# Performance work log

Hardware: AMD Instinct MI355X
Metric: run time of the kernel (lower is better)

## Reference

```python
import jax, jax.numpy as jnp
import numpy as np

NUM_EXPERTS = 8
IN_FEATURES = 1024
OUT_FEATURES = 1024
TOP_K = 2


def setup_inputs() -> dict:
    key = jax.random.key(0)
    k_x, k_we, k_be, k_wg, k_bg = jax.random.split(key, 5)
    scale_e = 1.0 / np.sqrt(IN_FEATURES)
    x = jax.random.normal(k_x, (4, 2048, IN_FEATURES), dtype=jnp.float32)
    # expert weights stored torch-style [E, out, in], bias [E, out]
    W_experts = jax.random.uniform(k_we, (NUM_EXPERTS, OUT_FEATURES, IN_FEATURES), minval=-scale_e, maxval=scale_e, dtype=jnp.float32)
    b_experts = jax.random.uniform(k_be, (NUM_EXPERTS, OUT_FEATURES), minval=-scale_e, maxval=scale_e, dtype=jnp.float32)
    W_gate = jax.random.uniform(k_wg, (NUM_EXPERTS, IN_FEATURES), minval=-scale_e, maxval=scale_e, dtype=jnp.float32)
    b_gate = jax.random.uniform(k_bg, (NUM_EXPERTS,), minval=-scale_e, maxval=scale_e, dtype=jnp.float32)
    return {"x": x, "W_experts": W_experts, "b_experts": b_experts, "W_gate": W_gate, "b_gate": b_gate}


def reference(x, W_experts, b_experts, W_gate, b_gate):
    B, S, D = x.shape
    x_flat = x.reshape(-1, D)  # [T, D]
    # gating
    gate_logits = x_flat @ W_gate.T + b_gate  # [T, E]
    topk_vals, topk_idxs = jax.lax.top_k(gate_logits, TOP_K)  # [T, K]
    topk_weights = jax.nn.softmax(topk_vals, axis=-1)  # [T, K]
    # dense per-token per-expert weight via one-hot scatter of top-k weights
    one_hot = jax.nn.one_hot(topk_idxs, NUM_EXPERTS, dtype=x.dtype)  # [T, K, E]
    w = jnp.einsum('tke,tk->te', one_hot, topk_weights)  # [T, E]
    # every expert runs densely over all tokens (faithful to source)
    expert_outs = jnp.einsum('td,efd->tef', x_flat, W_experts) + b_experts  # [T, E, F]
    out_flat = jnp.einsum('te,tef->tf', w, expert_outs)  # [T, F]
    return out_flat.reshape(B, S, -1)
```

## Files before the change

### kernel.cpp

```cpp
#include <hip/hip_runtime.h>
#include <hip/hip_bf16.h>
#include <stdint.h>

#define NE 8
#define DK 1024
#define FN 1024
#define NTOK 8192

#define BM 320
#define BN 256
#define BK 64
#define NIT (DK / BK)
#define MT 52

#define HB 32
#define EPB (NTOK * 2 / HB)

#define BUFS 73728
#define BOFF 40960

typedef __attribute__((ext_vector_type(4))) float f32x4;
typedef __attribute__((ext_vector_type(8))) short short8;
typedef __attribute__((ext_vector_type(4))) short short4v;

__device__ __forceinline__ unsigned short f2bf(float f) {
    union { float f; unsigned u; } v; v.f = f;
    unsigned r = v.u;
    unsigned lsb = (r >> 16) & 1u;
    r += 0x7fffu + lsb;
    return (unsigned short)(r >> 16);
}
__device__ __forceinline__ float bf2f(unsigned short u) {
    union { unsigned u; float f; } v; v.u = ((unsigned)u) << 16;
    return v.f;
}

__global__ __launch_bounds__(256) void k_gate(const float* __restrict__ x,
    const float* __restrict__ Wg, const float* __restrict__ bg,
    unsigned short* __restrict__ xb, int* __restrict__ meta_e,
    float* __restrict__ meta_w)
{
    const int lane = threadIdx.x & 63;
    const int t = blockIdx.x * 4 + (threadIdx.x >> 6);

    const f32x4* xr = (const f32x4*)(x + (size_t)t * DK);
    f32x4 xv[4];
#pragma unroll
    for (int c = 0; c < 4; ++c) xv[c] = xr[lane + 64 * c];

    short4v* xbo = (short4v*)(xb + (size_t)t * DK);
#pragma unroll
    for (int c = 0; c < 4; ++c) {
        short4v b;
        b.x = (short)f2bf(xv[c].x); b.y = (short)f2bf(xv[c].y);
        b.z = (short)f2bf(xv[c].z); b.w = (short)f2bf(xv[c].w);
        xbo[lane + 64 * c] = b;
    }

    float acc[NE];
#pragma unroll
    for (int e = 0; e < NE; ++e) {
        const f32x4* wr = (const f32x4*)(Wg + e * DK);
        float a = 0.f;
#pragma unroll
        for (int c = 0; c < 4; ++c) {
            f32x4 wv = wr[lane + 64 * c];
            a += xv[c].x * wv.x + xv[c].y * wv.y + xv[c].z * wv.z + xv[c].w * wv.w;
        }
        acc[e] = a;
    }
#pragma unroll
    for (int e = 0; e < NE; ++e) {
        float a = acc[e];
#pragma unroll
        for (int off = 32; off > 0; off >>= 1) a += __shfl_xor(a, off, 64);
        acc[e] = a;
    }
    if (lane == 0) {
        float v[NE];
#pragma unroll
        for (int e = 0; e < NE; ++e) v[e] = acc[e] + bg[e];
        int b0 = 0; float m0 = v[0];
#pragma unroll
        for (int e = 1; e < NE; ++e) if (v[e] > m0) { m0 = v[e]; b0 = e; }
        int b1 = -1; float m1 = -3.4e38f;
#pragma unroll
        for (int e = 0; e < NE; ++e) if (e != b0 && v[e] > m1) { m1 = v[e]; b1 = e; }
        float r = expf(m1 - m0);
        float s = 1.f + r;
        meta_e[2 * t] = b0; meta_e[2 * t + 1] = b1;
        meta_w[2 * t] = 1.f / s; meta_w[2 * t + 1] = r / s;
    }
}

__global__ __launch_bounds__(256) void k_convw(const float* __restrict__ W,
                                               unsigned short* __restrict__ Wb)
{
    int i = blockIdx.x * 256 + threadIdx.x;
    f32x4 v = ((const f32x4*)W)[i];
    short4v b;
    b.x = (short)f2bf(v.x); b.y = (short)f2bf(v.y);
    b.z = (short)f2bf(v.z); b.w = (short)f2bf(v.w);
    ((short4v*)Wb)[i] = b;
}

__global__ __launch_bounds__(256) void k_hist(const int* __restrict__ meta_e,
                                              int* __restrict__ blockcnt)
{
    __shared__ int lh[NE];
    if (threadIdx.x < NE) lh[threadIdx.x] = 0;
    __syncthreads();
    int base = blockIdx.x * EPB;
#pragma unroll
    for (int k = 0; k < EPB / 256; ++k)
        atomicAdd(&lh[meta_e[base + k * 256 + threadIdx.x]], 1);
    __syncthreads();
    if (threadIdx.x < NE) blockcnt[blockIdx.x * NE + threadIdx.x] = lh[threadIdx.x];
}

__global__ void k_scan(const int* __restrict__ blockcnt, int* __restrict__ seg,
                       int* __restrict__ base)
{
    __shared__ int pre[HB][NE];
    __shared__ int colsum[NE];
    __shared__ int segstart[NE];
    int tid = threadIdx.x;
    if (tid < NE) {
        int run = 0;
        for (int b = 0; b < HB; ++b) { pre[b][tid] = run; run += blockcnt[b * NE + tid]; }
        colsum[tid] = run;
    }
    __syncthreads();
    if (tid == 0) {
        int s = 0;
        for (int e = 0; e < NE; ++e) { segstart[e] = s; seg[e] = s; s += colsum[e]; }
        seg[NE] = s;
    }
    __syncthreads();
    for (int i = tid; i < HB * NE; i += 64) {
        int b = i / NE, e = i % NE;
        base[i] = segstart[e] + pre[b][e];
    }
}

__global__ __launch_bounds__(256) void k_scatter(const int* __restrict__ meta_e,
    const float* __restrict__ meta_w, const int* __restrict__ base,
    int* __restrict__ ridx, float* __restrict__ rw)
{
    __shared__ int lh[NE];
    __shared__ int bb[NE];
    if (threadIdx.x < NE) {
        lh[threadIdx.x] = 0;
        bb[threadIdx.x] = base[blockIdx.x * NE + threadIdx.x];
    }
    __syncthreads();
    int bs = blockIdx.x * EPB;
#pragma unroll
    for (int k = 0; k < EPB / 256; ++k) {
        int i = bs + k * 256 + threadIdx.x;
        int e = meta_e[i];
        int r = atomicAdd(&lh[e], 1);
        int p = bb[e] + r;
        ridx[p] = i;
        rw[p] = meta_w[i];
    }
}

template <int MODE>
__global__ __launch_bounds__(512, 2) void k_gemm(const unsigned short* __restrict__ xb,
    const unsigned short* __restrict__ Wb, const float* __restrict__ be,
    const int* __restrict__ seg, const int* __restrict__ ridx,
    const float* __restrict__ rw, float* __restrict__ out, void* __restrict__ ywv)
{
    __shared__ char Lds[2 * BUFS];

    const int bid = blockIdx.x;
    const int e = bid & 7;
    const int n0 = ((bid >> 3) & 3) * BN;
    const int mt = bid >> 5;
    const int s0 = seg[e];
    const int L = seg[e + 1] - s0;
    const int m0 = mt * BM;
    if (m0 >= L) return;

    const int tid = threadIdx.x;
    const int lane = tid & 63;
    const int wid = tid >> 6;
    const int wm = wid >> 2, wn = wid & 3;

    const int ag = ((tid & 7) ^ ((tid >> 3) & 7)) * 8;
    const unsigned short* asrc[5];
#pragma unroll
    for (int c = 0; c < 5; ++c) {
        int r = c * 64 + (tid >> 3);
        int idx = m0 + r; if (idx >= L) idx = L - 1;
        asrc[c] = xb + (size_t)(ridx[s0 + idx] >> 1) * DK + ag;
    }
    const int bgr = ((tid & 3) ^ ((tid >> 3) & 3)) * 8;
    const unsigned short* bsrc[2];
#pragma unroll
    for (int c = 0; c < 2; ++c) {
        int r = c * 128 + (tid >> 2);
        bsrc[c] = Wb + ((size_t)e * FN + n0 + r) * DK + bgr;
    }

    char* LB = (char*)Lds;

    f32x4 acc[10][4];
#pragma unroll
    for (int i = 0; i < 10; ++i)
#pragma unroll
        for (int j = 0; j < 4; ++j) acc[i][j] = f32x4{0.f, 0.f, 0.f, 0.f};

    const int frow = lane & 15;
    const int fq = lane >> 4;
    int a_off[10][2], b_off[4][2];
#pragma unroll
    for (int mi = 0; mi < 10; ++mi) {
        int r = wm * 160 + mi * 16 + frow;
#pragma unroll
        for (int kk = 0; kk < 2; ++kk)
            a_off[mi][kk] = r * 128 + (((kk * 4 + fq) ^ (r & 7)) * 16);
    }
#pragma unroll
    for (int ni = 0; ni < 4; ++ni) {
        int r = wn * 64 + ni * 16 + frow;
        int sl = fq ^ ((r >> 1) & 3);
#pragma unroll
        for (int kk = 0; kk < 2; ++kk)
            b_off[ni][kk] = BOFF + kk * 16384 + r * 64 + sl * 16;
    }

    auto STAGE_A = [&](int buf, int kt) {
        const int ko = kt * BK;
        char* dst = LB + buf * BUFS + wid * 1024;
#pragma unroll
        for (int c = 0; c < 5; ++c)
            __builtin_amdgcn_global_load_lds(
                (const __attribute__((address_space(1))) void*)(asrc[c] + ko),
                (__attribute__((address_space(3))) void*)(dst + c * 8192), 16, 0, 0);
    };
    auto STAGE_B = [&](int buf, int kt, int kh) {
        const int ko = kt * BK + kh * 32;
        char* dst = LB + buf * BUFS + BOFF + kh * 16384 + wid * 1024;
#pragma unroll
        for (int c = 0; c < 2; ++c)
            __builtin_amdgcn_global_load_lds(
                (const __attribute__((address_space(1))) void*)(bsrc[c] + ko),
                (__attribute__((address_space(3))) void*)(dst + c * 8192), 16, 0, 0);
    };

#define GATE2 do { asm volatile("s_waitcnt vmcnt(2)" ::: "memory"); \
                   __builtin_amdgcn_s_barrier(); \
                   __builtin_amdgcn_sched_barrier(0); } while (0)
#define GATE7 do { asm volatile("s_waitcnt vmcnt(7)" ::: "memory"); \
                   __builtin_amdgcn_s_barrier(); \
                   __builtin_amdgcn_sched_barrier(0); } while (0)
#define GATE0 do { asm volatile("s_waitcnt vmcnt(0)" ::: "memory"); \
                   __builtin_amdgcn_s_barrier(); \
                   __builtin_amdgcn_sched_barrier(0); } while (0)
#define BARP  do { __builtin_amdgcn_s_barrier(); \
                   __builtin_amdgcn_sched_barrier(0); } while (0)

#define CLUSTER(kk, mlo) do { \
    short8 bf4[4]; \
    _Pragma("unroll") \
    for (int ni = 0; ni < 4; ++ni) bf4[ni] = *(const short8*)(Cb + b_off[ni][kk]); \
    __builtin_amdgcn_s_setprio(1); \
    _Pragma("unroll") \
    for (int mi = (mlo); mi < (mlo) + 5; ++mi) { \
        short8 af = *(const short8*)(Cb + a_off[mi][kk]); \
        _Pragma("unroll") \
        for (int ni = 0; ni < 4; ++ni) \
            acc[mi][ni] = __builtin_amdgcn_mfma_f32_16x16x32_bf16( \
                af, bf4[ni], acc[mi][ni], 0, 0, 0); \
    } \
    __builtin_amdgcn_s_setprio(0); } while (0)

    STAGE_A(0, 0); STAGE_B(0, 0, 0); STAGE_B(0, 0, 1);
    __builtin_amdgcn_sched_barrier(0);

    for (int t = 0; t < NIT; ++t) {
        const int b = t & 1;
        const char* Cb = LB + b * BUFS;
        const bool st = (t + 1 < NIT);

        GATE2;
        if (st) STAGE_A(b ^ 1, t + 1);
        CLUSTER(0, 0);

        BARP;
        if (st) STAGE_B(b ^ 1, t + 1, 0);
        CLUSTER(0, 5);

        if (st) { GATE7; } else { GATE0; }
        if (st) STAGE_B(b ^ 1, t + 1, 1);
        CLUSTER(1, 0);

        BARP;
        CLUSTER(1, 5);
    }
#undef GATE2
#undef GATE7
#undef GATE0
#undef BARP
#undef CLUSTER

    float bias_n[4];
#pragma unroll
    for (int ni = 0; ni < 4; ++ni)
        bias_n[ni] = be[e * FN + n0 + wn * 64 + ni * 16 + frow];

    const int fq4 = fq * 4;
#pragma unroll
    for (int mi = 0; mi < 10; ++mi) {
        int rl = m0 + wm * 160 + mi * 16 + fq4;
#pragma unroll
        for (int j = 0; j < 4; ++j) {
            int idx = rl + j;
            if (idx < L) {
                float w = rw[s0 + idx];
                int oi = ridx[s0 + idx];
                if (MODE == 0) {
                    float* orow = out + (size_t)(oi >> 1) * FN + n0 + wn * 64 + frow;
#pragma unroll
                    for (int ni = 0; ni < 4; ++ni)
                        atomicAdd(orow + ni * 16, w * (acc[mi][ni][j] + bias_n[ni]));
                } else if (MODE == 1) {
                    unsigned short* yrow = (unsigned short*)ywv + (size_t)oi * FN + n0 + wn * 64 + frow;
#pragma unroll
                    for (int ni = 0; ni < 4; ++ni)
                        yrow[ni * 16] = f2bf(w * (acc[mi][ni][j] + bias_n[ni]));
                } else {
                    float* yrow = (float*)ywv + (size_t)oi * FN + n0 + wn * 64 + frow;
#pragma unroll
                    for (int ni = 0; ni < 4; ++ni)
                        yrow[ni * 16] = w * (acc[mi][ni][j] + bias_n[ni]);
                }
            }
        }
    }
}

__global__ __launch_bounds__(256) void k_combine_bf(const unsigned short* __restrict__ yw,
                                                    float* __restrict__ out)
{
    int t = blockIdx.x;
    const short4v* r0 = (const short4v*)(yw + (size_t)(2 * t) * FN);
    const short4v* r1 = (const short4v*)(yw + (size_t)(2 * t + 1) * FN);
    f32x4* o = (f32x4*)(out + (size_t)t * FN);
    int i = threadIdx.x;
    short4v a = r0[i], b = r1[i];
    f32x4 v;
    v.x = bf2f((unsigned short)a.x) + bf2f((unsigned short)b.x);
    v.y = bf2f((unsigned short)a.y) + bf2f((unsigned short)b.y);
    v.z = bf2f((unsigned short)a.z) + bf2f((unsigned short)b.z);
    v.w = bf2f((unsigned short)a.w) + bf2f((unsigned short)b.w);
    o[i] = v;
}

__global__ __launch_bounds__(256) void k_combine_f32(const float* __restrict__ yw,
                                                     float* __restrict__ out)
{
    int t = blockIdx.x;
    const f32x4* r0 = (const f32x4*)(yw + (size_t)(2 * t) * FN);
    const f32x4* r1 = (const f32x4*)(yw + (size_t)(2 * t + 1) * FN);
    f32x4* o = (f32x4*)(out + (size_t)t * FN);
    int i = threadIdx.x;
    o[i] = r0[i] + r1[i];
}

extern "C" void kernel_launch(void* const* d_in, const int* in_sizes, int n_in,
                              void* d_out, int out_size, void* d_ws, size_t ws_size,
                              hipStream_t stream)
{
    const float* x   = (const float*)d_in[0];
    const float* We  = (const float*)d_in[1];
    const float* beb = (const float*)d_in[2];
    const float* Wg  = (const float*)d_in[3];
    const float* bg  = (const float*)d_in[4];
    float* out = (float*)d_out;

    char* ws = (char*)d_ws;
    unsigned short* xb = (unsigned short*)ws;
    unsigned short* Wb = (unsigned short*)(ws + (size_t)(16 << 20));
    size_t off = (size_t)(32 << 20);
    int*   seg      = (int*)(ws + off);   off += 256;
    int*   blockcnt = (int*)(ws + off);   off += HB * NE * 4;
    int*   basebuf  = (int*)(ws + off);   off += HB * NE * 4;
    int*   meta_e   = (int*)(ws + off);   off += (size_t)NTOK * 2 * 4;
    float* meta_w   = (float*)(ws + off); off += (size_t)NTOK * 2 * 4;
    int*   ridxb    = (int*)(ws + off);   off += (size_t)NTOK * 2 * 4;
    float* rwb      = (float*)(ws + off); off += (size_t)NTOK * 2 * 4;
    void*  yw       = (void*)(ws + ((off + 255) & ~(size_t)255));
    size_t yw_base  = (size_t)((off + 255) & ~(size_t)255);

    int mode;
    if (ws_size >= yw_base + (size_t)NTOK * 2 * FN * 2) mode = 1;
    else if (ws_size >= yw_base + (size_t)NTOK * 2 * FN * 4) mode = 2;
    else mode = 0;

    k_gate<<<NTOK / 4, 256, 0, stream>>>(x, Wg, bg, xb, meta_e, meta_w);
    k_convw<<<(NE * FN * DK / 4) / 256, 256, 0, stream>>>(We, Wb);
    k_hist<<<HB, 256, 0, stream>>>(meta_e, blockcnt);
    k_scan<<<1, 64, 0, stream>>>(blockcnt, seg, basebuf);
    k_scatter<<<HB, 256, 0, stream>>>(meta_e, meta_w, basebuf, ridxb, rwb);

    const int nblk = NE * (FN / BN) * MT;
    if (mode == 1) {
        k_gemm<1><<<nblk, 512, 0, stream>>>(xb, Wb, beb, seg, ridxb, rwb, out, yw);
        k_combine_bf<<<NTOK, 256, 0, stream>>>((const unsigned short*)yw, out);
    } else if (mode == 2) {
        k_gemm<2><<<nblk, 512, 0, stream>>>(xb, Wb, beb, seg, ridxb, rwb, out, yw);
        k_combine_f32<<<NTOK, 256, 0, stream>>>((const float*)yw, out);
    } else {
        hipMemsetAsync(d_out, 0, (size_t)NTOK * FN * 4, stream);
        k_gemm<0><<<nblk, 512, 0, stream>>>(xb, Wb, beb, seg, ridxb, rwb, out, yw);
    }
}
```

Before: 89.70 us.

## Merge MFMA half-clusters per k-slice and vectorize permuted expert output stores

The main loop now loads all A and B fragments for a k-slice up front and issues the 40 MFMAs in one block. Previously each slice was split into two half-clusters separated by an extra barrier. This drops two barriers per iteration and issues staging loads earlier, at the cost of more live fragment registers. The expert epilogue writes four output columns per lane as one vector store in a permuted column order. The combine kernels undo that order through shared memory, trading scattered scalar stores for an extra LDS round trip.

```diff
diff --git a/kernel.cpp b/kernel.cpp
--- a/kernel.cpp
+++ b/kernel.cpp
@@ -250,32 +250,9 @@
                 (__attribute__((address_space(3))) void*)(dst + c * 8192), 16, 0, 0);
     };
 
-#define GATE2 do { asm volatile("s_waitcnt vmcnt(2)" ::: "memory"); \
-                   __builtin_amdgcn_s_barrier(); \
-                   __builtin_amdgcn_sched_barrier(0); } while (0)
-#define GATE7 do { asm volatile("s_waitcnt vmcnt(7)" ::: "memory"); \
-                   __builtin_amdgcn_s_barrier(); \
-                   __builtin_amdgcn_sched_barrier(0); } while (0)
-#define GATE0 do { asm volatile("s_waitcnt vmcnt(0)" ::: "memory"); \
-                   __builtin_amdgcn_s_barrier(); \
-                   __builtin_amdgcn_sched_barrier(0); } while (0)
-#define BARP  do { __builtin_amdgcn_s_barrier(); \
-                   __builtin_amdgcn_sched_barrier(0); } while (0)
-
-#define CLUSTER(kk, mlo) do { \
-    short8 bf4[4]; \
-    _Pragma("unroll") \
-    for (int ni = 0; ni < 4; ++ni) bf4[ni] = *(const short8*)(Cb + b_off[ni][kk]); \
-    __builtin_amdgcn_s_setprio(1); \
-    _Pragma("unroll") \
-    for (int mi = (mlo); mi < (mlo) + 5; ++mi) { \
-        short8 af = *(const short8*)(Cb + a_off[mi][kk]); \
-        _Pragma("unroll") \
-        for (int ni = 0; ni < 4; ++ni) \
-            acc[mi][ni] = __builtin_amdgcn_mfma_f32_16x16x32_bf16( \
-                af, bf4[ni], acc[mi][ni], 0, 0, 0); \
-    } \
-    __builtin_amdgcn_s_setprio(0); } while (0)
+#define GATE(N) do { asm volatile("s_waitcnt vmcnt(" #N ")" ::: "memory"); \
+                     __builtin_amdgcn_s_barrier(); \
+                     __builtin_amdgcn_sched_barrier(0); } while (0)
 
     STAGE_A(0, 0); STAGE_B(0, 0, 0); STAGE_B(0, 0, 1);
     __builtin_amdgcn_sched_barrier(0);
@@ -285,26 +262,39 @@
         const char* Cb = LB + b * BUFS;
         const bool st = (t + 1 < NIT);
 
-        GATE2;
-        if (st) STAGE_A(b ^ 1, t + 1);
-        CLUSTER(0, 0);
-
-        BARP;
-        if (st) STAGE_B(b ^ 1, t + 1, 0);
-        CLUSTER(0, 5);
-
-        if (st) { GATE7; } else { GATE0; }
+        GATE(2);
+        short8 b0f[4], a0f[10];
+#pragma unroll
+        for (int ni = 0; ni < 4; ++ni) b0f[ni] = *(const short8*)(Cb + b_off[ni][0]);
+#pragma unroll
+        for (int mi = 0; mi < 10; ++mi) a0f[mi] = *(const short8*)(Cb + a_off[mi][0]);
+        if (st) { STAGE_A(b ^ 1, t + 1); STAGE_B(b ^ 1, t + 1, 0); }
+        __builtin_amdgcn_s_setprio(1);
+#pragma unroll
+        for (int mi = 0; mi < 10; ++mi)
+#pragma unroll
+            for (int ni = 0; ni < 4; ++ni)
+                acc[mi][ni] = __builtin_amdgcn_mfma_f32_16x16x32_bf16(
+                    a0f[mi], b0f[ni], acc[mi][ni], 0, 0, 0);
+        __builtin_amdgcn_s_setprio(0);
+
+        if (st) { GATE(7); } else { GATE(0); }
+        short8 b1f[4], a1f[10];
+#pragma unroll
+        for (int ni = 0; ni < 4; ++ni) b1f[ni] = *(const short8*)(Cb + b_off[ni][1]);
+#pragma unroll
+        for (int mi = 0; mi < 10; ++mi) a1f[mi] = *(const short8*)(Cb + a_off[mi][1]);
         if (st) STAGE_B(b ^ 1, t + 1, 1);
-        CLUSTER(1, 0);
-
-        BARP;
-        CLUSTER(1, 5);
-    }
-#undef GATE2
-#undef GATE7
-#undef GATE0
-#undef BARP
-#undef CLUSTER
+        __builtin_amdgcn_s_setprio(1);
+#pragma unroll
+        for (int mi = 0; mi < 10; ++mi)
+#pragma unroll
+            for (int ni = 0; ni < 4; ++ni)
+                acc[mi][ni] = __builtin_amdgcn_mfma_f32_16x16x32_bf16(
+                    a1f[mi], b1f[ni], acc[mi][ni], 0, 0, 0);
+        __builtin_amdgcn_s_setprio(0);
+    }
+#undef GATE
 
     float bias_n[4];
 #pragma unroll
@@ -327,15 +317,19 @@
                     for (int ni = 0; ni < 4; ++ni)
                         atomicAdd(orow + ni * 16, w * (acc[mi][ni][j] + bias_n[ni]));
                 } else if (MODE == 1) {
-                    unsigned short* yrow = (unsigned short*)ywv + (size_t)oi * FN + n0 + wn * 64 + frow;
-#pragma unroll
-                    for (int ni = 0; ni < 4; ++ni)
-                        yrow[ni * 16] = f2bf(w * (acc[mi][ni][j] + bias_n[ni]));
+                    short4v pk;
+                    pk.x = (short)f2bf(w * (acc[mi][0][j] + bias_n[0]));
+                    pk.y = (short)f2bf(w * (acc[mi][1][j] + bias_n[1]));
+                    pk.z = (short)f2bf(w * (acc[mi][2][j] + bias_n[2]));
+                    pk.w = (short)f2bf(w * (acc[mi][3][j] + bias_n[3]));
+                    *(short4v*)((unsigned short*)ywv + (size_t)oi * FN + n0 + wn * 64 + frow * 4) = pk;
                 } else {
-                    float* yrow = (float*)ywv + (size_t)oi * FN + n0 + wn * 64 + frow;
-#pragma unroll
-                    for (int ni = 0; ni < 4; ++ni)
-                        yrow[ni * 16] = w * (acc[mi][ni][j] + bias_n[ni]);
+                    f32x4 pk;
+                    pk.x = w * (acc[mi][0][j] + bias_n[0]);
+                    pk.y = w * (acc[mi][1][j] + bias_n[1]);
+                    pk.z = w * (acc[mi][2][j] + bias_n[2]);
+                    pk.w = w * (acc[mi][3][j] + bias_n[3]);
+                    *(f32x4*)((float*)ywv + (size_t)oi * FN + n0 + wn * 64 + frow * 4) = pk;
                 }
             }
         }
@@ -345,29 +339,40 @@
 __global__ __launch_bounds__(256) void k_combine_bf(const unsigned short* __restrict__ yw,
                                                     float* __restrict__ out)
 {
-    int t = blockIdx.x;
-    const short4v* r0 = (const short4v*)(yw + (size_t)(2 * t) * FN);
-    const short4v* r1 = (const short4v*)(yw + (size_t)(2 * t + 1) * FN);
-    f32x4* o = (f32x4*)(out + (size_t)t * FN);
-    int i = threadIdx.x;
-    short4v a = r0[i], b = r1[i];
-    f32x4 v;
-    v.x = bf2f((unsigned short)a.x) + bf2f((unsigned short)b.x);
-    v.y = bf2f((unsigned short)a.y) + bf2f((unsigned short)b.y);
-    v.z = bf2f((unsigned short)a.z) + bf2f((unsigned short)b.z);
-    v.w = bf2f((unsigned short)a.w) + bf2f((unsigned short)b.w);
-    o[i] = v;
+    __shared__ float ls[FN];
+    int t = blockIdx.x, i = threadIdx.x;
+    const unsigned* r0 = (const unsigned*)(yw + (size_t)(2 * t) * FN);
+    const unsigned* r1 = (const unsigned*)(yw + (size_t)(2 * t + 1) * FN);
+    unsigned a0 = r0[2 * i], a1 = r0[2 * i + 1];
+    unsigned c0 = r1[2 * i], c1 = r1[2 * i + 1];
+    float s0 = bf2f((unsigned short)(a0 & 0xffff)) + bf2f((unsigned short)(c0 & 0xffff));
+    float s1 = bf2f((unsigned short)(a0 >> 16))    + bf2f((unsigned short)(c0 >> 16));
+    float s2 = bf2f((unsigned short)(a1 & 0xffff)) + bf2f((unsigned short)(c1 & 0xffff));
+    float s3 = bf2f((unsigned short)(a1 >> 16))    + bf2f((unsigned short)(c1 >> 16));
+    int base = (i >> 4) * 64 + (i & 15);
+    ls[base +  0] = s0;
+    ls[base + 16] = s1;
+    ls[base + 32] = s2;
+    ls[base + 48] = s3;
+    __syncthreads();
+    ((f32x4*)(out + (size_t)t * FN))[i] = ((const f32x4*)ls)[i];
 }
 
 __global__ __launch_bounds__(256) void k_combine_f32(const float* __restrict__ yw,
                                                      float* __restrict__ out)
 {
-    int t = blockIdx.x;
-    const f32x4* r0 = (const f32x4*)(yw + (size_t)(2 * t) * FN);
-    const f32x4* r1 = (const f32x4*)(yw + (size_t)(2 * t + 1) * FN);
-    f32x4* o = (f32x4*)(out + (size_t)t * FN);
-    int i = threadIdx.x;
-    o[i] = r0[i] + r1[i];
+    __shared__ float ls[FN];
+    int t = blockIdx.x, i = threadIdx.x;
+    f32x4 a = ((const f32x4*)(yw + (size_t)(2 * t) * FN))[i];
+    f32x4 b = ((const f32x4*)(yw + (size_t)(2 * t + 1) * FN))[i];
+    f32x4 s = a + b;
+    int base = (i >> 4) * 64 + (i & 15);
+    ls[base +  0] = s.x;
+    ls[base + 16] = s.y;
+    ls[base + 32] = s.z;
+    ls[base + 48] = s.w;
+    __syncthreads();
+    ((f32x4*)(out + (size_t)t * FN))[i] = ((const f32x4*)ls)[i];
 }
 
 extern "C" void kernel_launch(void* const* d_in, const int* in_sizes, int n_in,
```

Measured after the change: 87.94 us. -2.0%, faster.
